# Optimization experiments

Measured on AMD Instinct MI355X. Metric: run time of the kernel, lower is better.

The kernel has to match this reference:

```python
import jax, jax.numpy as jnp
import numpy as np

B, V, F, N = 4, 8192, 16384, 8192
EPS = 1e-3        # criterion eps
WEIGHT = 1000.0   # criterion weight


def setup_inputs() -> dict:
    key = jax.random.key(0)
    k1, k2, k3 = jax.random.split(key, 3)
    pred_pos = jax.random.normal(k1, (B, N, 3), jnp.float32)
    obstacle_pos = jax.random.normal(k2, (B, V, 3), jnp.float32)
    obstacle_faces = jax.random.randint(k3, (B, F, 3), 0, V)
    return {"pred_pos": pred_pos, "obstacle_pos": obstacle_pos,
            "obstacle_faces": obstacle_faces}


def _centers_normals(pos, faces):
    # pos: [V,3], faces: [F,3] -> face centers [F,3], unit face normals [F,3]
    tri = pos[faces]                                   # [F,3,3]
    centers = tri.mean(axis=1)                         # gather(...).mean(-2)
    n = jnp.cross(tri[:, 1] - tri[:, 0], tri[:, 2] - tri[:, 0])
    n = n / jnp.maximum(jnp.linalg.norm(n, axis=-1, keepdims=True), 1e-12)
    return centers, n


def reference(pred_pos, obstacle_pos, obstacle_faces):
    centers, normals = jax.vmap(_centers_normals)(obstacle_pos, obstacle_faces)
    # brute-force 1-NN: argmin_f ||p - c_f||^2 == argmin_f (||c_f||^2 - 2 p.c_f)
    c2 = jnp.sum(centers * centers, axis=-1)                     # [B,F]
    dots = jnp.einsum('bnd,bfd->bnf', pred_pos, centers)         # [B,N,F] big
    nn_idx = jnp.argmin(c2[:, None, :] - 2.0 * dots, axis=-1)    # [B,N]
    idx3 = jnp.broadcast_to(nn_idx[:, :, None], nn_idx.shape + (3,))
    nn_points = jnp.take_along_axis(centers, idx3, axis=1)       # [B,N,3]
    nn_normals = jnp.take_along_axis(normals, idx3, axis=1)      # [B,N,3]
    distance = jnp.sum((pred_pos - nn_points) * nn_normals, axis=-1)  # [B,N]
    interp = jnp.maximum(EPS - distance, 0.0)
    perc = jnp.mean((interp > 0).astype(jnp.float32))            # mean over B of per-example means (equal N)
    loss = jnp.mean(jnp.sum(interp ** 3, axis=-1)) * WEIGHT      # sum_i loss_i / B * weight
    return loss, perc
```

## Files before the change

### kernel.cpp

```cpp
#include <hip/hip_runtime.h>
#include <cstdint>

typedef __attribute__((ext_vector_type(8)))  short short8;
typedef __attribute__((ext_vector_type(16))) float floatx16;

constexpr int NB = 4;
constexpr int NV = 8192;
constexpr int NF = 16384;
constexpr int NP = 8192;
constexpr float F_EPS = 1e-3f;
constexpr float F_WEIGHT = 1000.0f;
constexpr float BIAS = 1e-3f;

constexpr int PT_TILES = NP / 32;
constexpr int FC_TILES = NF / 32;
constexpr int TPB = 256;
constexpr int FS = 16;
constexpr int SL_TILES = FC_TILES / FS;
constexpr int CH = 16;
constexpr int NCHUNK = SL_TILES / CH;
constexpr int PGB = 32;

union FragU { uint4 u; short8 s; };

__device__ inline unsigned f2bf(float f) {
    unsigned u = __float_as_uint(f);
    return (u + 0x7FFFu + ((u >> 16) & 1u)) >> 16;
}
__device__ inline float bf2f(unsigned h) { return __uint_as_float(h << 16); }
__device__ inline unsigned pk(unsigned lo, unsigned hi) {
    return (lo & 0xFFFFu) | (hi << 16);
}

__global__ void prep_kernel(const float* __restrict__ pred,
                            const float* __restrict__ pos,
                            const int*   __restrict__ faces,
                            uint4* __restrict__ a_frags,
                            uint4* __restrict__ b_frags,
                            float4* __restrict__ centers4,
                            float4* __restrict__ normals4,
                            unsigned* __restrict__ keys,
                            float* __restrict__ acc) {
    int i = blockIdx.x * blockDim.x + threadIdx.x;
    if (i >= NB * NF) return;
    if (i < 2) acc[i] = 0.0f;

    const unsigned ONE = 0x3F80u;

    {
        int b = i / NF, f = i & (NF - 1);
        const float* p = pos + (size_t)b * NV * 3;
        int i0 = faces[3 * (size_t)i], i1 = faces[3 * (size_t)i + 1], i2 = faces[3 * (size_t)i + 2];
        float ax = p[3 * i0], ay = p[3 * i0 + 1], az = p[3 * i0 + 2];
        float bx = p[3 * i1], by = p[3 * i1 + 1], bz = p[3 * i1 + 2];
        float cx = p[3 * i2], cy = p[3 * i2 + 1], cz = p[3 * i2 + 2];

        const float third = 1.0f / 3.0f;
        float mx = (ax + bx + cx) * third;
        float my = (ay + by + cy) * third;
        float mz = (az + bz + cz) * third;
        float c2 = mx * mx + my * my + mz * mz;

        float e1x = bx - ax, e1y = by - ay, e1z = bz - az;
        float e2x = cx - ax, e2y = cy - ay, e2z = cz - az;
        float nx = e1y * e2z - e1z * e2y;
        float ny = e1z * e2x - e1x * e2z;
        float nz = e1x * e2y - e1y * e2x;
        float len = sqrtf(nx * nx + ny * ny + nz * nz);
        float inv = 1.0f / fmaxf(len, 1e-12f);

        centers4[i] = make_float4(mx, my, mz, c2);
        normals4[i] = make_float4(nx * inv, ny * inv, nz * inv, 0.0f);

        unsigned bhx = f2bf(mx), bhy = f2bf(my), bhz = f2bf(mz);
        unsigned blx = f2bf(mx - bf2f(bhx)), bly = f2bf(my - bf2f(bhy)), blz = f2bf(mz - bf2f(bhz));
        unsigned c2h = f2bf(c2);
        unsigned c2l = f2bf(c2 - bf2f(c2h));

        int tile = f >> 5, n = f & 31;
        uint4* bb = b_frags + (size_t)(b * FC_TILES + tile) * 64;
        bb[n]      = make_uint4(pk(bhx, bhy), pk(bhz, bhx), pk(bhy, bhz), pk(blx, bly));
        bb[32 + n] = make_uint4(pk(blz, blx), pk(bly, blz), pk(c2h, c2l), pk(ONE, ONE));
    }

    if (i < NB * NP) {
        keys[i] = 0xFFFFFFFFu;
        int pb = i / NP, pn = i & (NP - 1);
        float x = pred[3 * (size_t)i], y = pred[3 * (size_t)i + 1], z = pred[3 * (size_t)i + 2];
        unsigned hx = f2bf(x), hy = f2bf(y), hz = f2bf(z);
        float rx = x - bf2f(hx), ry = y - bf2f(hy), rz = z - bf2f(hz);
        unsigned ahx = f2bf(-2.f * bf2f(hx)), ahy = f2bf(-2.f * bf2f(hy)), ahz = f2bf(-2.f * bf2f(hz));
        unsigned alx = f2bf(-2.f * rx), aly = f2bf(-2.f * ry), alz = f2bf(-2.f * rz);
        float p2 = x * x + y * y + z * z + BIAS;
        unsigned p2h = f2bf(p2);
        unsigned p2l = f2bf(p2 - bf2f(p2h));

        int tile = pn >> 5, m = pn & 31;
        uint4* ab = a_frags + (size_t)(pb * PT_TILES + tile) * 64;
        ab[m]      = make_uint4(pk(ahx, ahy), pk(ahz, alx), pk(aly, alz), pk(ahx, ahy));
        ab[32 + m] = make_uint4(pk(ahz, alx), pk(aly, alz), pk(ONE, ONE), pk(p2h, p2l));
    }
}

__global__ __launch_bounds__(TPB) void nn_kernel(
        const uint4* __restrict__ a_frags,
        const uint4* __restrict__ b_frags,
        unsigned* __restrict__ keys) {
    const int pg = blockIdx.x, sl = blockIdx.y, b = blockIdx.z;
    const int tid = threadIdx.x, wave = tid >> 6, lane = tid & 63;

    __shared__ uint4 sb[CH * 64];

    const int t0 = pg * 8 + wave * 2;
    FragU a0, a1;
    a0.u = a_frags[((size_t)(b * PT_TILES + t0)) * 64 + lane];
    a1.u = a_frags[((size_t)(b * PT_TILES + t0 + 1)) * 64 + lane];

    unsigned best0[16], best1[16];
#pragma unroll
    for (int e = 0; e < 16; ++e) { best0[e] = 0xFFFFFFFFu; best1[e] = 0xFFFFFFFFu; }

    const floatx16 zero = {0.f, 0.f, 0.f, 0.f, 0.f, 0.f, 0.f, 0.f,
                           0.f, 0.f, 0.f, 0.f, 0.f, 0.f, 0.f, 0.f};
    const uint4* bp = b_frags + ((size_t)(b * FC_TILES + sl * SL_TILES)) * 64;

    for (int ch = 0; ch < NCHUNK; ++ch) {
        const uint4* gsrc = bp + (size_t)ch * CH * 64;
        __syncthreads();
#pragma unroll
        for (int k = 0; k < (CH * 64) / TPB; ++k)
            sb[k * TPB + tid] = gsrc[k * TPB + tid];
        __syncthreads();

        unsigned vf = (unsigned)((sl * SL_TILES + ch * CH) * 32 + (lane & 31));
#pragma unroll
        for (int t = 0; t < CH; t += 2) {
            FragU fb0, fb1;
            fb0.u = sb[t * 64 + lane];
            fb1.u = sb[t * 64 + 64 + lane];
            floatx16 d00 = __builtin_amdgcn_mfma_f32_32x32x16_bf16(a0.s, fb0.s, zero, 0, 0, 0);
            floatx16 d01 = __builtin_amdgcn_mfma_f32_32x32x16_bf16(a0.s, fb1.s, zero, 0, 0, 0);
#pragma unroll
            for (int r = 0; r < 16; ++r) {
                unsigned k0 = (__float_as_uint(d00[r]) & 0xFFFFC000u) | vf;
                unsigned k1 = (__float_as_uint(d01[r]) & 0xFFFFC000u) | (vf + 32u);
                best0[r] = min(best0[r], min(k0, k1));
            }
            floatx16 d10 = __builtin_amdgcn_mfma_f32_32x32x16_bf16(a1.s, fb0.s, zero, 0, 0, 0);
            floatx16 d11 = __builtin_amdgcn_mfma_f32_32x32x16_bf16(a1.s, fb1.s, zero, 0, 0, 0);
#pragma unroll
            for (int r = 0; r < 16; ++r) {
                unsigned k0 = (__float_as_uint(d10[r]) & 0xFFFFC000u) | vf;
                unsigned k1 = (__float_as_uint(d11[r]) & 0xFFFFC000u) | (vf + 32u);
                best1[r] = min(best1[r], min(k0, k1));
            }
            vf += 64u;
        }
    }

#pragma unroll
    for (int e = 0; e < 16; ++e) {
        unsigned v0 = best0[e], v1 = best1[e];
#pragma unroll
        for (int m = 1; m < 32; m <<= 1) {
            v0 = min(v0, (unsigned)__shfl_xor((int)v0, m, 64));
            v1 = min(v1, (unsigned)__shfl_xor((int)v1, m, 64));
        }
        best0[e] = v0; best1[e] = v1;
    }
    unsigned* kb = keys + b * NP;
    if ((lane & 31) == 0) {
        int half = lane >> 5;
#pragma unroll
        for (int r = 0; r < 16; ++r) {
            int row = (r & 3) + 8 * (r >> 2) + 4 * half;
            atomicMin(&kb[t0 * 32 + row], best0[r]);
            atomicMin(&kb[(t0 + 1) * 32 + row], best1[r]);
        }
    }
}

__global__ __launch_bounds__(TPB) void finalize_kernel(
        const float* __restrict__ pred,
        const float4* __restrict__ centers4,
        const float4* __restrict__ normals4,
        const unsigned int* __restrict__ keys,
        float* __restrict__ acc) {
    int i = blockIdx.x * blockDim.x + threadIdx.x;
    float val = 0.0f, cnt = 0.0f;
    if (i < NB * NP) {
        int b = i / NP;
        unsigned key = keys[i];
        int idx = (int)(key & (unsigned)(NF - 1));
        float4 c  = centers4[b * NF + idx];
        float4 nr = normals4[b * NF + idx];
        const float* pp = pred + (size_t)i * 3;
        float dx = pp[0] - c.x, dy = pp[1] - c.y, dz = pp[2] - c.z;
        float dist = dx * nr.x + dy * nr.y + dz * nr.z;
        float t = F_EPS - dist;
        if (t > 0.0f) { cnt = 1.0f; val = t * t * t; }
    }
    for (int off = 32; off > 0; off >>= 1) {
        val += __shfl_down(val, off, 64);
        cnt += __shfl_down(cnt, off, 64);
    }
    __shared__ float sv[TPB / 64], sn[TPB / 64];
    int lane = threadIdx.x & 63, wave = threadIdx.x >> 6;
    if (lane == 0) { sv[wave] = val; sn[wave] = cnt; }
    __syncthreads();
    if (threadIdx.x == 0) {
        float v = 0.0f, cc = 0.0f;
#pragma unroll
        for (int w = 0; w < TPB / 64; ++w) { v += sv[w]; cc += sn[w]; }
        atomicAdd(&acc[0], v);
        atomicAdd(&acc[1], cc);
    }
}

__global__ void out_kernel(const float* __restrict__ acc,
                           float* __restrict__ out) {
    if (threadIdx.x == 0) {
        out[0] = acc[0] * (F_WEIGHT / (float)NB);
        out[1] = acc[1] * (1.0f / (float)(NB * NP));
    }
}

extern "C" void kernel_launch(void* const* d_in, const int* in_sizes, int n_in,
                              void* d_out, int out_size, void* d_ws, size_t ws_size,
                              hipStream_t stream) {
    const float* pred  = (const float*)d_in[0];
    const float* opos  = (const float*)d_in[1];
    const int*   faces = (const int*)  d_in[2];

    char* ws = (char*)d_ws;
    const size_t a_bytes = (size_t)NB * PT_TILES * 64 * 16;
    const size_t b_bytes = (size_t)NB * FC_TILES * 64 * 16;
    const size_t c_bytes = (size_t)NB * NF * 16;
    const size_t k_bytes = (size_t)NB * NP * sizeof(unsigned);

    uint4*    a_frags  = (uint4*)ws;
    uint4*    b_frags  = (uint4*)(ws + a_bytes);
    float4*   centers4 = (float4*)(ws + a_bytes + b_bytes);
    float4*   normals4 = (float4*)(ws + a_bytes + b_bytes + c_bytes);
    unsigned* keys     = (unsigned*)(ws + a_bytes + b_bytes + 2 * c_bytes);
    float*    acc      = (float*)(ws + a_bytes + b_bytes + 2 * c_bytes + k_bytes);

    prep_kernel<<<(NB * NF + TPB - 1) / TPB, TPB, 0, stream>>>(
        pred, opos, faces, a_frags, b_frags, centers4, normals4, keys, acc);

    nn_kernel<<<dim3(PGB, FS, NB), TPB, 0, stream>>>(a_frags, b_frags, keys);

    finalize_kernel<<<(NB * NP + TPB - 1) / TPB, TPB, 0, stream>>>(
        pred, centers4, normals4, keys, acc);

    out_kernel<<<1, 64, 0, stream>>>(acc, (float*)d_out);
}
```

Measured before the change: 113.4 us.

## Use one point tile per wave, double grid, fuse output into finalize

Each wave in the nearest-neighbour kernel now owns one 32-point tile instead of two. The number of point-group blocks is doubled to keep the same coverage, which halves per-thread accumulator registers and aims for higher occupancy. The MFMA pair is emitted through inline assembly with explicit s_nop padding. The separate out kernel is removed: the last finalize block, found through an atomic ticket counter, writes the scaled outputs, saving one launch. The costs are twice as many shared-memory face-tile loads across blocks and hand-coded hazard nops that may over-stall the pipeline.

Result: no change. 113.2 us (-0.1%).

```diff
diff --git a/kernel.cpp b/kernel.cpp
--- a/kernel.cpp
+++ b/kernel.cpp
@@ -19,7 +19,7 @@
 constexpr int SL_TILES = FC_TILES / FS;
 constexpr int CH = 16;
 constexpr int NCHUNK = SL_TILES / CH;
-constexpr int PGB = 32;
+constexpr int PGB = 64;
 
 union FragU { uint4 u; short8 s; };
 
@@ -40,10 +40,12 @@
                             float4* __restrict__ centers4,
                             float4* __restrict__ normals4,
                             unsigned* __restrict__ keys,
-                            float* __restrict__ acc) {
+                            float* __restrict__ acc,
+                            unsigned* __restrict__ tk) {
     int i = blockIdx.x * blockDim.x + threadIdx.x;
     if (i >= NB * NF) return;
     if (i < 2) acc[i] = 0.0f;
+    if (i == 0) tk[0] = 0u;
 
     const unsigned ONE = 0x3F80u;
 
@@ -111,14 +113,13 @@
 
     __shared__ uint4 sb[CH * 64];
 
-    const int t0 = pg * 8 + wave * 2;
-    FragU a0, a1;
-    a0.u = a_frags[((size_t)(b * PT_TILES + t0)) * 64 + lane];
-    a1.u = a_frags[((size_t)(b * PT_TILES + t0 + 1)) * 64 + lane];
-
-    unsigned best0[16], best1[16];
-#pragma unroll
-    for (int e = 0; e < 16; ++e) { best0[e] = 0xFFFFFFFFu; best1[e] = 0xFFFFFFFFu; }
+    const int pt_tile = pg * 4 + wave;
+    FragU a;
+    a.u = a_frags[((size_t)(b * PT_TILES + pt_tile)) * 64 + lane];
+
+    unsigned best[16];
+#pragma unroll
+    for (int e = 0; e < 16; ++e) best[e] = 0xFFFFFFFFu;
 
     const floatx16 zero = {0.f, 0.f, 0.f, 0.f, 0.f, 0.f, 0.f, 0.f,
                            0.f, 0.f, 0.f, 0.f, 0.f, 0.f, 0.f, 0.f};
@@ -138,21 +139,18 @@
             FragU fb0, fb1;
             fb0.u = sb[t * 64 + lane];
             fb1.u = sb[t * 64 + 64 + lane];
-            floatx16 d00 = __builtin_amdgcn_mfma_f32_32x32x16_bf16(a0.s, fb0.s, zero, 0, 0, 0);
-            floatx16 d01 = __builtin_amdgcn_mfma_f32_32x32x16_bf16(a0.s, fb1.s, zero, 0, 0, 0);
+            floatx16 d0, d1;
+            asm("v_mfma_f32_32x32x16_bf16 %0, %2, %3, %5\n\t"
+                "v_mfma_f32_32x32x16_bf16 %1, %2, %4, %5\n\t"
+                "s_nop 7\n\t"
+                "s_nop 7"
+                : "=&v"(d0), "=&v"(d1)
+                : "v"(a.s), "v"(fb0.s), "v"(fb1.s), "v"(zero));
 #pragma unroll
             for (int r = 0; r < 16; ++r) {
-                unsigned k0 = (__float_as_uint(d00[r]) & 0xFFFFC000u) | vf;
-                unsigned k1 = (__float_as_uint(d01[r]) & 0xFFFFC000u) | (vf + 32u);
-                best0[r] = min(best0[r], min(k0, k1));
-            }
-            floatx16 d10 = __builtin_amdgcn_mfma_f32_32x32x16_bf16(a1.s, fb0.s, zero, 0, 0, 0);
-            floatx16 d11 = __builtin_amdgcn_mfma_f32_32x32x16_bf16(a1.s, fb1.s, zero, 0, 0, 0);
-#pragma unroll
-            for (int r = 0; r < 16; ++r) {
-                unsigned k0 = (__float_as_uint(d10[r]) & 0xFFFFC000u) | vf;
-                unsigned k1 = (__float_as_uint(d11[r]) & 0xFFFFC000u) | (vf + 32u);
-                best1[r] = min(best1[r], min(k0, k1));
+                unsigned k0 = (__float_as_uint(d0[r]) & 0xFFFFC000u) | vf;
+                unsigned k1 = (__float_as_uint(d1[r]) & 0xFFFFC000u) | (vf + 32u);
+                best[r] = min(best[r], min(k0, k1));
             }
             vf += 64u;
         }
@@ -160,13 +158,11 @@
 
 #pragma unroll
     for (int e = 0; e < 16; ++e) {
-        unsigned v0 = best0[e], v1 = best1[e];
-#pragma unroll
-        for (int m = 1; m < 32; m <<= 1) {
-            v0 = min(v0, (unsigned)__shfl_xor((int)v0, m, 64));
-            v1 = min(v1, (unsigned)__shfl_xor((int)v1, m, 64));
-        }
-        best0[e] = v0; best1[e] = v1;
+        unsigned v = best[e];
+#pragma unroll
+        for (int m = 1; m < 32; m <<= 1)
+            v = min(v, (unsigned)__shfl_xor((int)v, m, 64));
+        best[e] = v;
     }
     unsigned* kb = keys + b * NP;
     if ((lane & 31) == 0) {
@@ -174,8 +170,7 @@
 #pragma unroll
         for (int r = 0; r < 16; ++r) {
             int row = (r & 3) + 8 * (r >> 2) + 4 * half;
-            atomicMin(&kb[t0 * 32 + row], best0[r]);
-            atomicMin(&kb[(t0 + 1) * 32 + row], best1[r]);
+            atomicMin(&kb[pt_tile * 32 + row], best[r]);
         }
     }
 }
@@ -185,7 +180,10 @@
         const float4* __restrict__ centers4,
         const float4* __restrict__ normals4,
         const unsigned int* __restrict__ keys,
-        float* __restrict__ acc) {
+        float* __restrict__ acc,
+        unsigned* __restrict__ tk,
+        float* __restrict__ out,
+        int nblocks) {
     int i = blockIdx.x * blockDim.x + threadIdx.x;
     float val = 0.0f, cnt = 0.0f;
     if (i < NB * NP) {
@@ -205,6 +203,7 @@
         cnt += __shfl_down(cnt, off, 64);
     }
     __shared__ float sv[TPB / 64], sn[TPB / 64];
+    __shared__ unsigned s_tkt;
     int lane = threadIdx.x & 63, wave = threadIdx.x >> 6;
     if (lane == 0) { sv[wave] = val; sn[wave] = cnt; }
     __syncthreads();
@@ -214,14 +213,14 @@
         for (int w = 0; w < TPB / 64; ++w) { v += sv[w]; cc += sn[w]; }
         atomicAdd(&acc[0], v);
         atomicAdd(&acc[1], cc);
-    }
-}
-
-__global__ void out_kernel(const float* __restrict__ acc,
-                           float* __restrict__ out) {
-    if (threadIdx.x == 0) {
-        out[0] = acc[0] * (F_WEIGHT / (float)NB);
-        out[1] = acc[1] * (1.0f / (float)(NB * NP));
+        __threadfence();
+        s_tkt = atomicAdd(&tk[0], 1u);
+        if (s_tkt == (unsigned)(nblocks - 1)) {
+            float a0 = __hip_atomic_load(&acc[0], __ATOMIC_RELAXED, __HIP_MEMORY_SCOPE_AGENT);
+            float a1 = __hip_atomic_load(&acc[1], __ATOMIC_RELAXED, __HIP_MEMORY_SCOPE_AGENT);
+            out[0] = a0 * (F_WEIGHT / (float)NB);
+            out[1] = a1 * (1.0f / (float)(NB * NP));
+        }
     }
 }
 
@@ -244,14 +243,14 @@
     float4*   normals4 = (float4*)(ws + a_bytes + b_bytes + c_bytes);
     unsigned* keys     = (unsigned*)(ws + a_bytes + b_bytes + 2 * c_bytes);
     float*    acc      = (float*)(ws + a_bytes + b_bytes + 2 * c_bytes + k_bytes);
+    unsigned* tk       = (unsigned*)(ws + a_bytes + b_bytes + 2 * c_bytes + k_bytes + 64);
 
     prep_kernel<<<(NB * NF + TPB - 1) / TPB, TPB, 0, stream>>>(
-        pred, opos, faces, a_frags, b_frags, centers4, normals4, keys, acc);
+        pred, opos, faces, a_frags, b_frags, centers4, normals4, keys, acc, tk);
 
     nn_kernel<<<dim3(PGB, FS, NB), TPB, 0, stream>>>(a_frags, b_frags, keys);
 
-    finalize_kernel<<<(NB * NP + TPB - 1) / TPB, TPB, 0, stream>>>(
-        pred, centers4, normals4, keys, acc);
-
-    out_kernel<<<1, 64, 0, stream>>>(acc, (float*)d_out);
-}
+    int fin_blocks = (NB * NP + TPB - 1) / TPB;
+    finalize_kernel<<<fin_blocks, TPB, 0, stream>>>(
+        pred, centers4, normals4, keys, acc, tk, (float*)d_out, fin_blocks);
+}
```
